# Performance work log

Measured on AMD Instinct MI355X. Metric: run time of the kernel, lower is better.

Reference implementation:

```python
import jax, jax.numpy as jnp
import numpy as np

B, N, T, M, D, H = 2, 2048, 8, 256, 1024, 16
HD = D // H
EPS = 1e-5


def setup_inputs() -> dict:
    key = jax.random.key(0)
    ks = jax.random.split(key, 12)
    text_tokens = jax.random.normal(ks[0], (B, N, D), dtype=jnp.float32)
    media = jax.random.normal(ks[1], (B, T, M, D), dtype=jnp.float32)
    # exactly T media markers, evenly spaced, first at position 0 so no
    # fully-masked softmax row (matches well-formed usage of the module)
    loc = np.zeros((B, N), dtype=bool)
    loc[:, (np.arange(T) * (N // T))] = True
    media_locations = jnp.asarray(loc)
    s = 0.02
    return {
        "text_tokens": text_tokens,
        "media": media,
        "media_locations": media_locations,
        "ln_gamma": jnp.ones((D,), jnp.float32),
        "ln_beta": jnp.zeros((D,), jnp.float32),
        "wq": jax.random.normal(ks[2], (D, D), jnp.float32) * s,
        "wk": jax.random.normal(ks[3], (D, D), jnp.float32) * s,
        "wv": jax.random.normal(ks[4], (D, D), jnp.float32) * s,
        "bq": jnp.zeros((D,), jnp.float32),
        "bk": jnp.zeros((D,), jnp.float32),
        "bv": jnp.zeros((D,), jnp.float32),
        "w_out": jax.random.normal(ks[5], (D, D), jnp.float32) * s,
        "b_out": jnp.zeros((D,), jnp.float32),
    }


def _layernorm(x, gamma, beta):
    mu = jnp.mean(x, axis=-1, keepdims=True)
    var = jnp.mean(jnp.square(x - mu), axis=-1, keepdims=True)
    return (x - mu) * jax.lax.rsqrt(var + EPS) * gamma + beta


def reference(text_tokens, media, media_locations, ln_gamma, ln_beta,
              wq, wk, wv, bq, bk, bv, w_out, b_out):
    b, t, m, d = media.shape
    n = text_tokens.shape[1]
    h, hd = H, HD

    x = _layernorm(text_tokens, ln_gamma, ln_beta)          # [b,n,d]
    kv = media.reshape(b, t * m, d)                          # [b,tm,d]

    q = (x @ wq + bq).reshape(b, n, h, hd)
    k = (kv @ wk + bk).reshape(b, t * m, h, hd)
    v = (kv @ wv + bv).reshape(b, t * m, h, hd)

    scale = 1.0 / jnp.sqrt(jnp.asarray(hd, jnp.float32))
    scores = jnp.einsum('bnhk,bshk->bhns', q, k) * scale     # [b,h,n,tm]

    # media-locality mask: text token attends only to its immediately
    # preceding media frame (cumsum of media_locations == frame index)
    text_cumsum = jnp.cumsum(media_locations.astype(jnp.int32), axis=-1)  # [b,n]
    media_nums = jnp.repeat(jnp.arange(1, t + 1, dtype=jnp.int32), m)     # [tm]
    allowed = text_cumsum[:, :, None] == media_nums[None, None, :]        # [b,n,tm]
    scores = jnp.where(allowed[:, None, :, :], scores, -jnp.inf)

    attn = jax.nn.softmax(scores, axis=-1)                   # [b,h,n,tm]
    out = jnp.einsum('bhns,bshk->bnhk', attn, v).reshape(b, n, d)
    return out @ w_out + b_out
```

## Files before the change

kernel.cpp:

```cpp
#include <hip/hip_runtime.h>
#include <hip/hip_fp16.h>


typedef _Float16 h8 __attribute__((ext_vector_type(8)));
typedef _Float16 h4 __attribute__((ext_vector_type(4)));
typedef float f4 __attribute__((ext_vector_type(4)));

#define DI __device__ __forceinline__

DI void gload16(const void* g, void* l) {
  __builtin_amdgcn_global_load_lds((const __attribute__((address_space(1))) unsigned int*)g,
                                   (__attribute__((address_space(3))) unsigned int*)l, 16, 0, 0);
}

__global__ __launch_bounds__(256) void ln_cast_kernel(const float* __restrict__ x,
    const float* __restrict__ gamma, const float* __restrict__ beta, _Float16* __restrict__ xh) {
  int row = blockIdx.x;
  int tid = threadIdx.x;
  const f4* xr = (const f4*)(x + (size_t)row * 1024);
  f4 v = xr[tid];
  float s = v[0] + v[1] + v[2] + v[3];
  float ss = v[0]*v[0] + v[1]*v[1] + v[2]*v[2] + v[3]*v[3];
  #pragma unroll
  for (int m = 1; m < 64; m <<= 1) { s += __shfl_xor(s, m); ss += __shfl_xor(ss, m); }
  __shared__ float red[8];
  int wid = tid >> 6, lane = tid & 63;
  if (lane == 0) { red[wid] = s; red[4 + wid] = ss; }
  __syncthreads();
  s = red[0] + red[1] + red[2] + red[3];
  ss = red[4] + red[5] + red[6] + red[7];
  float mean = s * (1.0f / 1024.0f);
  float var = ss * (1.0f / 1024.0f) - mean * mean;
  float rs = rsqrtf(var + 1e-5f);
  const f4* gr = (const f4*)gamma;
  const f4* br = (const f4*)beta;
  f4 g = gr[tid], be = br[tid];
  h4 o;
  #pragma unroll
  for (int j = 0; j < 4; ++j) o[j] = (_Float16)((v[j] - mean) * rs * g[j] + be[j]);
  ((h4*)(xh + (size_t)row * 1024))[tid] = o;
}

__global__ __launch_bounds__(256) void cast_kernel(const float* __restrict__ in,
    _Float16* __restrict__ out, int n4) {
  int i = blockIdx.x * 256 + threadIdx.x;
  if (i < n4) {
    f4 v = ((const f4*)in)[i];
    h4 o;
    #pragma unroll
    for (int j = 0; j < 4; ++j) o[j] = (_Float16)v[j];
    ((h4*)out)[i] = o;
  }
}

__global__ __launch_bounds__(256) void transpose_cast_kernel(const float* __restrict__ W0,
    const float* __restrict__ W1, const float* __restrict__ W2, const float* __restrict__ W3,
    _Float16* __restrict__ Wt) {
  const float* W = blockIdx.z == 0 ? W0 : blockIdx.z == 1 ? W1 : blockIdx.z == 2 ? W2 : W3;
  _Float16* out = Wt + (size_t)blockIdx.z * 1024 * 1024;
  __shared__ float tile[32][33];
  int i0 = blockIdx.x * 32, o0 = blockIdx.y * 32;
  int tx = threadIdx.x & 31, ty = threadIdx.x >> 5;
  #pragma unroll
  for (int r = 0; r < 4; ++r)
    tile[ty + r * 8][tx] = W[(size_t)(i0 + ty + r * 8) * 1024 + o0 + tx];
  __syncthreads();
  #pragma unroll
  for (int r = 0; r < 4; ++r)
    out[(size_t)(o0 + ty + r * 8) * 1024 + i0 + tx] = (_Float16)tile[tx][ty + r * 8];
}

__global__ __launch_bounds__(64) void build_qlist_kernel(const int* __restrict__ locs,
    int* __restrict__ cnt, int* __restrict__ qlist) {
  int b = blockIdx.x, lane = threadIdx.x;
  __shared__ int lcnt[8];
  if (lane < 8) lcnt[lane] = 0;
  __syncthreads();
  int run = 0; int v[32];
  #pragma unroll
  for (int i = 0; i < 32; ++i) { run += locs[b * 2048 + lane * 32 + i]; v[i] = run; }
  int incl = run;
  #pragma unroll
  for (int d = 1; d < 64; d <<= 1) { int t = __shfl_up(incl, d); if (lane >= d) incl += t; }
  int excl = incl - run;
  #pragma unroll
  for (int i = 0; i < 32; ++i) {
    int c = excl + v[i];
    if (c >= 1 && c <= 8) {
      int pos = atomicAdd(&lcnt[c - 1], 1);
      qlist[(b * 8 + (c - 1)) * 2048 + pos] = lane * 32 + i;
    }
  }
  __syncthreads();
  if (lane < 8) cnt[b * 8 + lane] = lcnt[lane];
}

struct GemmDesc { const _Float16* A; const _Float16* Bt; const float* bias; void* C; int mode; };
struct GemmBatch { GemmDesc d[3]; };

__global__ __launch_bounds__(512) void gemm128(GemmBatch gb) {
  GemmDesc g = gb.d[blockIdx.z];
  int row0 = blockIdx.y * 128, col0 = blockIdx.x * 128;
  __shared__ alignas(16) _Float16 As[128 * 32];
  __shared__ alignas(16) _Float16 Bs[128 * 32];
  int tid = threadIdx.x, lane = tid & 63, wid = tid >> 6;
  int wr = wid >> 2, wc = wid & 3;
  f4 acc[4][2] = {};
  int r_st = wid * 16 + (lane >> 2);
  int c_st = lane & 3;
  int cg = c_st ^ ((r_st >> 1) & 3);
  const _Float16* gA = g.A + (size_t)(row0 + r_st) * 1024 + cg * 8;
  const _Float16* gB = g.Bt + (size_t)(col0 + r_st) * 1024 + cg * 8;
  int cb = lane >> 4;
  #pragma unroll 1
  for (int kt = 0; kt < 32; ++kt) {
    __syncthreads();
    gload16(gA + kt * 32, (void*)&As[wid * 512]);
    gload16(gB + kt * 32, (void*)&Bs[wid * 512]);
    __syncthreads();
    h8 af[4], bf[2];
    #pragma unroll
    for (int m = 0; m < 4; ++m) {
      int r = wr * 64 + m * 16 + (lane & 15);
      af[m] = *(const h8*)&As[r * 32 + ((cb ^ ((r >> 1) & 3)) * 8)];
    }
    #pragma unroll
    for (int n = 0; n < 2; ++n) {
      int r = wc * 32 + n * 16 + (lane & 15);
      bf[n] = *(const h8*)&Bs[r * 32 + ((cb ^ ((r >> 1) & 3)) * 8)];
    }
    #pragma unroll
    for (int m = 0; m < 4; ++m)
      #pragma unroll
      for (int n = 0; n < 2; ++n)
        acc[m][n] = __builtin_amdgcn_mfma_f32_16x16x32_f16(af[m], bf[n], acc[m][n], 0, 0, 0);
  }
  int colb = col0 + wc * 32;
  float bias_v[2];
  #pragma unroll
  for (int n = 0; n < 2; ++n) bias_v[n] = g.bias[colb + n * 16 + (lane & 15)];
  #pragma unroll
  for (int m = 0; m < 4; ++m) {
    int row = row0 + wr * 64 + m * 16 + (lane >> 4) * 4;
    #pragma unroll
    for (int n = 0; n < 2; ++n) {
      int col = colb + n * 16 + (lane & 15);
      if (g.mode == 0) {
        _Float16* C = (_Float16*)g.C;
        #pragma unroll
        for (int j = 0; j < 4; ++j)
          C[(size_t)(row + j) * 1024 + col] = (_Float16)(acc[m][n][j] + bias_v[n]);
      } else if (g.mode == 1) {
        float* C = (float*)g.C;
        #pragma unroll
        for (int j = 0; j < 4; ++j)
          C[(size_t)(row + j) * 1024 + col] = acc[m][n][j] + bias_v[n];
      } else {
        _Float16* C = (_Float16*)g.C;
        h4 pk;
        #pragma unroll
        for (int j = 0; j < 4; ++j) pk[j] = (_Float16)(acc[m][n][j] + bias_v[n]);
        size_t vrow = (size_t)((row >> 11) * 1024 + col);
        *(h4*)&C[vrow * 2048 + (row & 2047)] = pk;
      }
    }
  }
}

__global__ __launch_bounds__(512) void attn_kernel(const _Float16* __restrict__ Qg,
    const _Float16* __restrict__ Kg, const _Float16* __restrict__ Vtg,
    const int* __restrict__ cnt, const int* __restrict__ qlist, _Float16* __restrict__ Og) {
  int h = blockIdx.x, f = blockIdx.y, b = blockIdx.z;
  __shared__ alignas(16) _Float16 Kl[256 * 64];
  __shared__ alignas(16) _Float16 Vl[64 * 256];
  __shared__ alignas(16) _Float16 Sl[8 * 16 * 256];
  int tid = threadIdx.x;
  for (int idx = tid; idx < 2048; idx += 512) {
    int r = idx >> 3, c = idx & 7;
    h8 v = *(const h8*)&Kg[((size_t)(b * 2048 + f * 256 + r)) * 1024 + h * 64 + c * 8];
    *(h8*)&Kl[r * 64 + ((c ^ (r & 7)) * 8)] = v;
  }
  for (int idx = tid; idx < 2048; idx += 512) {
    int d = idx >> 5, cc = idx & 31;
    h8 v = *(const h8*)&Vtg[((size_t)(b * 1024 + h * 64 + d)) * 2048 + f * 256 + cc * 8];
    *(h8*)&Vl[d * 256 + ((cc ^ (d & 7)) * 8)] = v;
  }
  __syncthreads();
  int nq = cnt[b * 8 + f];
  int lane = tid & 63, wid = tid >> 6;
  const int* ql = qlist + (b * 8 + f) * 2048;
  _Float16* Sw = &Sl[wid * 4096];
  for (int st = wid; st * 16 < nq; st += 8) {
    int qbase = st * 16;
    int nv = nq - qbase; if (nv > 16) nv = 16;
    int li = lane & 15; if (li > nv - 1) li = nv - 1;
    int qrow = b * 2048 + ql[qbase + li];
    h8 aq0 = *(const h8*)&Qg[(size_t)qrow * 1024 + h * 64 + (lane >> 4) * 8];
    h8 aq1 = *(const h8*)&Qg[(size_t)qrow * 1024 + h * 64 + 32 + (lane >> 4) * 8];
    f4 s[16];
    #pragma unroll
    for (int kt = 0; kt < 16; ++kt) {
      int key = kt * 16 + (lane & 15);
      int cb0 = lane >> 4;
      h8 bk0 = *(const h8*)&Kl[key * 64 + ((cb0 ^ (key & 7)) * 8)];
      h8 bk1 = *(const h8*)&Kl[key * 64 + (((cb0 + 4) ^ (key & 7)) * 8)];
      f4 z = {0.f, 0.f, 0.f, 0.f};
      s[kt] = __builtin_amdgcn_mfma_f32_16x16x32_f16(aq0, bk0, z, 0, 0, 0);
      s[kt] = __builtin_amdgcn_mfma_f32_16x16x32_f16(aq1, bk1, s[kt], 0, 0, 0);
    }
    float mx[4], sm[4];
    #pragma unroll
    for (int j = 0; j < 4; ++j) {
      float m = s[0][j];
      #pragma unroll
      for (int kt = 1; kt < 16; ++kt) m = fmaxf(m, s[kt][j]);
      #pragma unroll
      for (int d = 1; d < 16; d <<= 1) m = fmaxf(m, __shfl_xor(m, d));
      mx[j] = m; sm[j] = 0.f;
    }
    #pragma unroll
    for (int kt = 0; kt < 16; ++kt) {
      int keyb = kt * 16 + (lane & 15);
      int cbk = keyb >> 3, wi = keyb & 7;
      #pragma unroll
      for (int j = 0; j < 4; ++j) {
        float p = __expf((s[kt][j] - mx[j]) * 0.125f);
        sm[j] += p;
        int q = (lane >> 4) * 4 + j;
        Sw[q * 256 + ((cbk ^ (q & 7)) * 8) + wi] = (_Float16)p;
      }
    }
    #pragma unroll
    for (int j = 0; j < 4; ++j) {
      float x = sm[j];
      #pragma unroll
      for (int d = 1; d < 16; d <<= 1) x += __shfl_xor(x, d);
      sm[j] = x;
    }
    f4 o[4] = {};
    #pragma unroll
    for (int c32 = 0; c32 < 8; ++c32) {
      int qa = lane & 15;
      int cba = c32 * 4 + (lane >> 4);
      h8 pa = *(const h8*)&Sw[qa * 256 + ((cba ^ (qa & 7)) * 8)];
      #pragma unroll
      for (int dt = 0; dt < 4; ++dt) {
        int dd = dt * 16 + (lane & 15);
        h8 bv_ = *(const h8*)&Vl[dd * 256 + ((cba ^ (dd & 7)) * 8)];
        o[dt] = __builtin_amdgcn_mfma_f32_16x16x32_f16(pa, bv_, o[dt], 0, 0, 0);
      }
    }
    #pragma unroll
    for (int j = 0; j < 4; ++j) {
      int q = (lane >> 4) * 4 + j;
      if (q < nv) {
        int qr = __shfl(qrow, q);
        float inv = 1.0f / sm[j];
        #pragma unroll
        for (int dt = 0; dt < 4; ++dt)
          Og[(size_t)qr * 1024 + h * 64 + dt * 16 + (lane & 15)] = (_Float16)(o[dt][j] * inv);
      }
    }
  }
}

extern "C" void kernel_launch(void* const* d_in, const int* in_sizes, int n_in,
                              void* d_out, int out_size, void* d_ws, size_t ws_size,
                              hipStream_t stream) {
  const float* text  = (const float*)d_in[0];
  const float* media = (const float*)d_in[1];
  const int*   locs  = (const int*)d_in[2];
  const float* gamma = (const float*)d_in[3];
  const float* beta  = (const float*)d_in[4];
  const float* wq = (const float*)d_in[5];
  const float* wk = (const float*)d_in[6];
  const float* wv = (const float*)d_in[7];
  const float* bq = (const float*)d_in[8];
  const float* bk = (const float*)d_in[9];
  const float* bv = (const float*)d_in[10];
  const float* wo = (const float*)d_in[11];
  const float* bo = (const float*)d_in[12];

  char* ws = (char*)d_ws;
  size_t off = 0;
  auto take = [&](size_t bytes) { void* p = ws + off; off += (bytes + 255) & ~(size_t)255; return p; };
  _Float16* xh  = (_Float16*)take((size_t)4096 * 1024 * 2);
  _Float16* kvh = (_Float16*)take((size_t)4096 * 1024 * 2);
  _Float16* wt  = (_Float16*)take((size_t)4 * 1024 * 1024 * 2);
  _Float16* Qm  = (_Float16*)take((size_t)4096 * 1024 * 2);
  _Float16* Km  = (_Float16*)take((size_t)4096 * 1024 * 2);
  _Float16* Vt  = (_Float16*)take((size_t)2048 * 2048 * 2);
  _Float16* Om  = (_Float16*)take((size_t)4096 * 1024 * 2);
  int* cnt   = (int*)take(64 * sizeof(int));
  int* qlist = (int*)take((size_t)2 * 8 * 2048 * sizeof(int));

  ln_cast_kernel<<<4096, 256, 0, stream>>>(text, gamma, beta, xh);
  cast_kernel<<<4096, 256, 0, stream>>>(media, kvh, 1048576);
  transpose_cast_kernel<<<dim3(32, 32, 4), 256, 0, stream>>>(wq, wk, wv, wo, wt);
  build_qlist_kernel<<<2, 64, 0, stream>>>(locs, cnt, qlist);

  GemmBatch gb;
  gb.d[0] = { xh,  wt,                       bq, (void*)Qm, 0 };
  gb.d[1] = { kvh, wt + (size_t)1 * 1048576, bk, (void*)Km, 0 };
  gb.d[2] = { kvh, wt + (size_t)2 * 1048576, bv, (void*)Vt, 2 };
  gemm128<<<dim3(8, 32, 3), 512, 0, stream>>>(gb);

  attn_kernel<<<dim3(16, 8, 2), 512, 0, stream>>>(Qm, Km, Vt, cnt, qlist, Om);

  GemmBatch gf;
  gf.d[0] = { Om, wt + (size_t)3 * 1048576, bo, d_out, 1 };
  gf.d[1] = gf.d[0];
  gf.d[2] = gf.d[0];
  gemm128<<<dim3(8, 32, 1), 512, 0, stream>>>(gf);
}
```

Before: 195.7 us.

## Merge preprocessing kernels into one launch and deepen GEMM K-tile to 64

The four preprocessing kernels (layernorm cast, media cast, weight transpose-cast, query-list build) are combined into a single launch that dispatches on block index, removing three launch gaps. The GEMM now stages a 64-wide K slice per iteration instead of 32, with a matching XOR swizzle, which halves the number of loop iterations and barrier pairs. The cost is double the shared memory per block, which may reduce occupancy. The heterogeneous fused launch also forces every block to reserve the shared memory of the largest branch.

Result: no change. 192.5 us (-1.6%).

```diff
diff --git a/kernel.cpp b/kernel.cpp
--- a/kernel.cpp
+++ b/kernel.cpp
@@ -13,86 +13,85 @@
                                    (__attribute__((address_space(3))) unsigned int*)l, 16, 0, 0);
 }
 
-__global__ __launch_bounds__(256) void ln_cast_kernel(const float* __restrict__ x,
-    const float* __restrict__ gamma, const float* __restrict__ beta, _Float16* __restrict__ xh) {
-  int row = blockIdx.x;
+__global__ __launch_bounds__(256) void prep_kernel(
+    const float* __restrict__ x, const float* __restrict__ gamma, const float* __restrict__ beta,
+    _Float16* __restrict__ xh,
+    const float* __restrict__ media, _Float16* __restrict__ kvh,
+    const float* __restrict__ W0, const float* __restrict__ W1,
+    const float* __restrict__ W2, const float* __restrict__ W3, _Float16* __restrict__ Wt,
+    const int* __restrict__ locs, int* __restrict__ cnt, int* __restrict__ qlist) {
+  int bid = blockIdx.x;
   int tid = threadIdx.x;
-  const f4* xr = (const f4*)(x + (size_t)row * 1024);
-  f4 v = xr[tid];
-  float s = v[0] + v[1] + v[2] + v[3];
-  float ss = v[0]*v[0] + v[1]*v[1] + v[2]*v[2] + v[3]*v[3];
-  #pragma unroll
-  for (int m = 1; m < 64; m <<= 1) { s += __shfl_xor(s, m); ss += __shfl_xor(ss, m); }
-  __shared__ float red[8];
-  int wid = tid >> 6, lane = tid & 63;
-  if (lane == 0) { red[wid] = s; red[4 + wid] = ss; }
-  __syncthreads();
-  s = red[0] + red[1] + red[2] + red[3];
-  ss = red[4] + red[5] + red[6] + red[7];
-  float mean = s * (1.0f / 1024.0f);
-  float var = ss * (1.0f / 1024.0f) - mean * mean;
-  float rs = rsqrtf(var + 1e-5f);
-  const f4* gr = (const f4*)gamma;
-  const f4* br = (const f4*)beta;
-  f4 g = gr[tid], be = br[tid];
-  h4 o;
-  #pragma unroll
-  for (int j = 0; j < 4; ++j) o[j] = (_Float16)((v[j] - mean) * rs * g[j] + be[j]);
-  ((h4*)(xh + (size_t)row * 1024))[tid] = o;
-}
-
-__global__ __launch_bounds__(256) void cast_kernel(const float* __restrict__ in,
-    _Float16* __restrict__ out, int n4) {
-  int i = blockIdx.x * 256 + threadIdx.x;
-  if (i < n4) {
-    f4 v = ((const f4*)in)[i];
+  if (bid < 4096) {
+    int row = bid;
+    const f4* xr = (const f4*)(x + (size_t)row * 1024);
+    f4 v = xr[tid];
+    float s = v[0] + v[1] + v[2] + v[3];
+    float ss = v[0]*v[0] + v[1]*v[1] + v[2]*v[2] + v[3]*v[3];
+    #pragma unroll
+    for (int m = 1; m < 64; m <<= 1) { s += __shfl_xor(s, m); ss += __shfl_xor(ss, m); }
+    __shared__ float red[8];
+    int wid = tid >> 6, lane = tid & 63;
+    if (lane == 0) { red[wid] = s; red[4 + wid] = ss; }
+    __syncthreads();
+    s = red[0] + red[1] + red[2] + red[3];
+    ss = red[4] + red[5] + red[6] + red[7];
+    float mean = s * (1.0f / 1024.0f);
+    float var = ss * (1.0f / 1024.0f) - mean * mean;
+    float rs = rsqrtf(var + 1e-5f);
+    f4 g = ((const f4*)gamma)[tid], be = ((const f4*)beta)[tid];
     h4 o;
     #pragma unroll
+    for (int j = 0; j < 4; ++j) o[j] = (_Float16)((v[j] - mean) * rs * g[j] + be[j]);
+    ((h4*)(xh + (size_t)row * 1024))[tid] = o;
+  } else if (bid < 8192) {
+    int i = (bid - 4096) * 256 + tid;
+    f4 v = ((const f4*)media)[i];
+    h4 o;
+    #pragma unroll
     for (int j = 0; j < 4; ++j) o[j] = (_Float16)v[j];
-    ((h4*)out)[i] = o;
-  }
-}
-
-__global__ __launch_bounds__(256) void transpose_cast_kernel(const float* __restrict__ W0,
-    const float* __restrict__ W1, const float* __restrict__ W2, const float* __restrict__ W3,
-    _Float16* __restrict__ Wt) {
-  const float* W = blockIdx.z == 0 ? W0 : blockIdx.z == 1 ? W1 : blockIdx.z == 2 ? W2 : W3;
-  _Float16* out = Wt + (size_t)blockIdx.z * 1024 * 1024;
-  __shared__ float tile[32][33];
-  int i0 = blockIdx.x * 32, o0 = blockIdx.y * 32;
-  int tx = threadIdx.x & 31, ty = threadIdx.x >> 5;
-  #pragma unroll
-  for (int r = 0; r < 4; ++r)
-    tile[ty + r * 8][tx] = W[(size_t)(i0 + ty + r * 8) * 1024 + o0 + tx];
-  __syncthreads();
-  #pragma unroll
-  for (int r = 0; r < 4; ++r)
-    out[(size_t)(o0 + ty + r * 8) * 1024 + i0 + tx] = (_Float16)tile[tx][ty + r * 8];
-}
-
-__global__ __launch_bounds__(64) void build_qlist_kernel(const int* __restrict__ locs,
-    int* __restrict__ cnt, int* __restrict__ qlist) {
-  int b = blockIdx.x, lane = threadIdx.x;
-  __shared__ int lcnt[8];
-  if (lane < 8) lcnt[lane] = 0;
-  __syncthreads();
-  int run = 0; int v[32];
-  #pragma unroll
-  for (int i = 0; i < 32; ++i) { run += locs[b * 2048 + lane * 32 + i]; v[i] = run; }
-  int incl = run;
-  #pragma unroll
-  for (int d = 1; d < 64; d <<= 1) { int t = __shfl_up(incl, d); if (lane >= d) incl += t; }
-  int excl = incl - run;
-  #pragma unroll
-  for (int i = 0; i < 32; ++i) {
-    int c = excl + v[i];
-    if (c >= 1 && c <= 8) {
-      int pos = atomicAdd(&lcnt[c - 1], 1);
-      qlist[(b * 8 + (c - 1)) * 2048 + pos] = lane * 32 + i;
-    }
-  }
-  __syncthreads();
-  if (lane < 8) cnt[b * 8 + lane] = lcnt[lane];
+    ((h4*)kvh)[i] = o;
+  } else if (bid < 12288) {
+    int sec = bid - 8192;
+    int z = sec >> 10, r = sec & 1023;
+    const float* W = z == 0 ? W0 : z == 1 ? W1 : z == 2 ? W2 : W3;
+    _Float16* out = Wt + (size_t)z * 1024 * 1024;
+    __shared__ float tile[32][33];
+    int i0 = (r & 31) * 32, o0 = (r >> 5) * 32;
+    int tx = tid & 31, ty = tid >> 5;
+    #pragma unroll
+    for (int rr = 0; rr < 4; ++rr)
+      tile[ty + rr * 8][tx] = W[(size_t)(i0 + ty + rr * 8) * 1024 + o0 + tx];
+    __syncthreads();
+    #pragma unroll
+    for (int rr = 0; rr < 4; ++rr)
+      out[(size_t)(o0 + ty + rr * 8) * 1024 + i0 + tx] = (_Float16)tile[tx][ty + rr * 8];
+  } else {
+    int b = bid - 12288;
+    __shared__ int lcnt[8];
+    if (tid < 8) lcnt[tid] = 0;
+    __syncthreads();
+    if (tid < 64) {
+      int lane = tid;
+      int run = 0; int v[32];
+      #pragma unroll
+      for (int i = 0; i < 32; ++i) { run += locs[b * 2048 + lane * 32 + i]; v[i] = run; }
+      int incl = run;
+      #pragma unroll
+      for (int d = 1; d < 64; d <<= 1) { int t = __shfl_up(incl, d); if (lane >= d) incl += t; }
+      int excl = incl - run;
+      #pragma unroll
+      for (int i = 0; i < 32; ++i) {
+        int c = excl + v[i];
+        if (c >= 1 && c <= 8) {
+          int pos = atomicAdd(&lcnt[c - 1], 1);
+          qlist[(b * 8 + (c - 1)) * 2048 + pos] = lane * 32 + i;
+        }
+      }
+    }
+    __syncthreads();
+    if (tid < 8) cnt[b * 8 + tid] = lcnt[tid];
+  }
 }
 
 struct GemmDesc { const _Float16* A; const _Float16* Bt; const float* bias; void* C; int mode; };
@@ -101,39 +100,50 @@
 __global__ __launch_bounds__(512) void gemm128(GemmBatch gb) {
   GemmDesc g = gb.d[blockIdx.z];
   int row0 = blockIdx.y * 128, col0 = blockIdx.x * 128;
-  __shared__ alignas(16) _Float16 As[128 * 32];
-  __shared__ alignas(16) _Float16 Bs[128 * 32];
+  __shared__ alignas(16) _Float16 As[128 * 64];
+  __shared__ alignas(16) _Float16 Bs[128 * 64];
   int tid = threadIdx.x, lane = tid & 63, wid = tid >> 6;
   int wr = wid >> 2, wc = wid & 3;
   f4 acc[4][2] = {};
-  int r_st = wid * 16 + (lane >> 2);
-  int c_st = lane & 3;
-  int cg = c_st ^ ((r_st >> 1) & 3);
-  const _Float16* gA = g.A + (size_t)(row0 + r_st) * 1024 + cg * 8;
-  const _Float16* gB = g.Bt + (size_t)(col0 + r_st) * 1024 + cg * 8;
-  int cb = lane >> 4;
+  int r0s = tid >> 3, c0s = tid & 7;
+  int cg0 = c0s ^ (r0s & 7);
+  int r1s = r0s + 64;
+  int cg1 = c0s ^ (r1s & 7);
+  const _Float16* gA0 = g.A + (size_t)(row0 + r0s) * 1024 + cg0 * 8;
+  const _Float16* gA1 = g.A + (size_t)(row0 + r1s) * 1024 + cg1 * 8;
+  const _Float16* gB0 = g.Bt + (size_t)(col0 + r0s) * 1024 + cg0 * 8;
+  const _Float16* gB1 = g.Bt + (size_t)(col0 + r1s) * 1024 + cg1 * 8;
   #pragma unroll 1
-  for (int kt = 0; kt < 32; ++kt) {
-    __syncthreads();
-    gload16(gA + kt * 32, (void*)&As[wid * 512]);
-    gload16(gB + kt * 32, (void*)&Bs[wid * 512]);
-    __syncthreads();
-    h8 af[4], bf[2];
-    #pragma unroll
-    for (int m = 0; m < 4; ++m) {
-      int r = wr * 64 + m * 16 + (lane & 15);
-      af[m] = *(const h8*)&As[r * 32 + ((cb ^ ((r >> 1) & 3)) * 8)];
-    }
-    #pragma unroll
-    for (int n = 0; n < 2; ++n) {
-      int r = wc * 32 + n * 16 + (lane & 15);
-      bf[n] = *(const h8*)&Bs[r * 32 + ((cb ^ ((r >> 1) & 3)) * 8)];
-    }
-    #pragma unroll
-    for (int m = 0; m < 4; ++m)
-      #pragma unroll
-      for (int n = 0; n < 2; ++n)
-        acc[m][n] = __builtin_amdgcn_mfma_f32_16x16x32_f16(af[m], bf[n], acc[m][n], 0, 0, 0);
+  for (int kt = 0; kt < 16; ++kt) {
+    __syncthreads();
+    gload16(gA0 + kt * 64, (void*)&As[wid * 512]);
+    gload16(gA1 + kt * 64, (void*)&As[4096 + wid * 512]);
+    gload16(gB0 + kt * 64, (void*)&Bs[wid * 512]);
+    gload16(gB1 + kt * 64, (void*)&Bs[4096 + wid * 512]);
+    __syncthreads();
+    h8 af[2][4], bf[2][2];
+    #pragma unroll
+    for (int kk = 0; kk < 2; ++kk) {
+      #pragma unroll
+      for (int m = 0; m < 4; ++m) {
+        int r = wr * 64 + m * 16 + (lane & 15);
+        int c = ((lane >> 4) + kk * 4) ^ (r & 7);
+        af[kk][m] = *(const h8*)&As[r * 64 + c * 8];
+      }
+      #pragma unroll
+      for (int n = 0; n < 2; ++n) {
+        int r = wc * 32 + n * 16 + (lane & 15);
+        int c = ((lane >> 4) + kk * 4) ^ (r & 7);
+        bf[kk][n] = *(const h8*)&Bs[r * 64 + c * 8];
+      }
+    }
+    #pragma unroll
+    for (int kk = 0; kk < 2; ++kk)
+      #pragma unroll
+      for (int m = 0; m < 4; ++m)
+        #pragma unroll
+        for (int n = 0; n < 2; ++n)
+          acc[m][n] = __builtin_amdgcn_mfma_f32_16x16x32_f16(af[kk][m], bf[kk][n], acc[m][n], 0, 0, 0);
   }
   int colb = col0 + wc * 32;
   float bias_v[2];
@@ -294,10 +304,8 @@
   int* cnt   = (int*)take(64 * sizeof(int));
   int* qlist = (int*)take((size_t)2 * 8 * 2048 * sizeof(int));
 
-  ln_cast_kernel<<<4096, 256, 0, stream>>>(text, gamma, beta, xh);
-  cast_kernel<<<4096, 256, 0, stream>>>(media, kvh, 1048576);
-  transpose_cast_kernel<<<dim3(32, 32, 4), 256, 0, stream>>>(wq, wk, wv, wo, wt);
-  build_qlist_kernel<<<2, 64, 0, stream>>>(locs, cnt, qlist);
+  prep_kernel<<<12290, 256, 0, stream>>>(text, gamma, beta, xh, media, kvh,
+                                         wq, wk, wv, wo, wt, locs, cnt, qlist);
 
   GemmBatch gb;
   gb.d[0] = { xh,  wt,                       bq, (void*)Qm, 0 };
```
